# Optimization experiments

Hardware: AMD Instinct MI355X
Metric: run time of the kernel (lower is better)

## Reference

```python
import jax, jax.numpy as jnp
import numpy as np

D_MODEL = 1024
NUM_HEADS = 16
D_HEAD = D_MODEL // NUM_HEADS
EPS = 1e-06


def setup_inputs() -> dict:
    key = jax.random.key(0)
    ks = jax.random.split(key, 11)
    B, T = 16, 8192
    s = 1.0 / np.sqrt(D_MODEL)
    inp = {
        "query": jax.random.normal(ks[0], (B, 1, D_MODEL), jnp.float32),
        "key": jax.random.normal(ks[1], (B, T, D_MODEL), jnp.float32),
        "value": jax.random.normal(ks[2], (B, T, D_MODEL), jnp.float32),
        "Wq": jax.random.normal(ks[3], (D_MODEL, D_MODEL), jnp.float32) * s,
        "bq": jnp.zeros((D_MODEL,), jnp.float32),
        "Wk": jax.random.normal(ks[4], (D_MODEL, D_MODEL), jnp.float32) * s,
        "bk": jnp.zeros((D_MODEL,), jnp.float32),
        "Wv": jax.random.normal(ks[5], (D_MODEL, D_MODEL), jnp.float32) * s,
        "bv": jnp.zeros((D_MODEL,), jnp.float32),
        "Wo": jax.random.normal(ks[6], (D_MODEL, D_MODEL), jnp.float32) * s,
        "bo": jnp.zeros((D_MODEL,), jnp.float32),
    }
    return inp


def _feature_map(x):
    # ELU + 1 ensures positivity
    return jax.nn.elu(x) + 1.0


def reference(query, key, value, Wq, bq, Wk, bk, Wv, bv, Wo, bo):
    B, T, _ = key.shape
    H, dh = NUM_HEADS, D_HEAD
    # projections (torch Linear: x @ W^T + b)
    Q = (query @ Wq.T + bq).reshape(B, 1, H, dh).transpose(0, 2, 1, 3)  # [B,H,1,dh]
    K = (key @ Wk.T + bk).reshape(B, T, H, dh).transpose(0, 2, 1, 3)    # [B,H,T,dh]
    V = (value @ Wv.T + bv).reshape(B, T, H, dh).transpose(0, 2, 1, 3)  # [B,H,T,dh]
    Q = _feature_map(Q)
    K = _feature_map(K)
    # linear-attention accumulators
    KV = jnp.einsum("bhtd,bhte->bhde", K, V)        # [B,H,dh,dh]
    Z = K.sum(axis=2)                                  # [B,H,dh]
    num = jnp.einsum("bhqd,bhde->bhqe", Q, KV)       # [B,H,1,dh]
    den = jnp.einsum("bhqd,bhd->bhq", Q, Z)[..., None]  # [B,H,1,1]
    out = num / (den + EPS)
    out = out.transpose(0, 2, 1, 3).reshape(B, 1, D_MODEL)
    return out @ Wo.T + bo
```

## Files before the change

### kernel.cpp

```cpp
#include <hip/hip_runtime.h>


typedef __attribute__((ext_vector_type(8))) short  bf16x8;
typedef __attribute__((ext_vector_type(4))) short  bf16x4;
typedef __attribute__((ext_vector_type(4))) float  f32x4;

#define WS_QPHI 0u
#define WS_PRE  65536u
#define WS_S    131072u
#define WS_WKB  1179648u
#define WS_W    3276800u

__device__ __forceinline__ unsigned short f2bf(float f) {
  union { float f; unsigned u; } c; c.f = f;
  unsigned u = c.u;
  return (unsigned short)((u + 0x7fffu + ((u >> 16) & 1u)) >> 16);
}

__device__ __forceinline__ void gload_lds16(const void* g, void* l) {
  __builtin_amdgcn_global_load_lds((const __attribute__((address_space(1))) void*)g,
                                   (__attribute__((address_space(3))) void*)l, 16, 0, 0);
}

__global__ void k_convert_wk(const float* __restrict__ Wk, unsigned short* __restrict__ Wkb) {
  int i = blockIdx.x * 256 + threadIdx.x;
  f32x4 v = ((const f32x4*)Wk)[i];
  bf16x4 o;
  o[0] = (short)f2bf(v[0]); o[1] = (short)f2bf(v[1]);
  o[2] = (short)f2bf(v[2]); o[3] = (short)f2bf(v[3]);
  ((bf16x4*)Wkb)[i] = o;
}

__global__ void k_qproj(const float* __restrict__ q, const float* __restrict__ Wq,
                        const float* __restrict__ bq, float* __restrict__ Qphi) {
  int b = blockIdx.x, h = blockIdx.y, d = threadIdx.x;
  const f32x4* qr = (const f32x4*)(q + b * 1024);
  const f32x4* wr = (const f32x4*)(Wq + (size_t)(h * 64 + d) * 1024);
  float s = bq[h * 64 + d];
  for (int i = 0; i < 256; ++i) {
    f32x4 a = qr[i], ww = wr[i];
    s += a[0]*ww[0] + a[1]*ww[1] + a[2]*ww[2] + a[3]*ww[3];
  }
  s = s > 0.f ? s + 1.f : __expf(s);
  Qphi[(b * 16 + h) * 64 + d] = s;
}

__global__ __launch_bounds__(512)
void k_kproj(const float* __restrict__ key, const unsigned short* __restrict__ Wkb,
             const float* __restrict__ bk, const float* __restrict__ Qphi,
             float* __restrict__ w) {
  __shared__ unsigned short sA[2][128 * 40];
  __shared__ unsigned short sB[2][256 * 32];

  const int bid  = blockIdx.x + (blockIdx.y << 2);
  const int work = ((bid & 7) << 9) | (bid >> 3);
  const int np   = work & 3;
  const int mb   = work >> 2;
  const int b    = mb >> 6;
  const int mrow = (mb & 63) << 7;
  const int tid  = threadIdx.x;
  const int lane = tid & 63;
  const int wv   = tid >> 6;
  const int wr   = wv >> 2;
  const int wc   = wv & 3;
  const int n0   = np << 8;
  const int h    = (np << 2) | wc;
  const int l15  = lane & 15;
  const int lk   = (lane >> 4) << 3;

  const int ar = tid >> 2, aq = tid & 3;
  const float* Ab = key + ((size_t)((b << 13) + mrow + ar)) * 1024 + aq * 8;
  const int sAoff = ar * 40 + aq * 8;

  const int bsw = ((lane & 3) ^ ((lane >> 3) & 3)) << 3;
  const unsigned short* Bb = Wkb + ((size_t)(n0 + (wv << 5) + (lane >> 2))) * 1024 + bsw;

  f32x4 acc[4][4];
  #pragma unroll
  for (int i = 0; i < 4; ++i)
    #pragma unroll
    for (int j = 0; j < 4; ++j) acc[i][j] = (f32x4)0.f;

  float qreg[4];
  #pragma unroll
  for (int ni = 0; ni < 4; ++ni)
    qreg[ni] = Qphi[((b << 4) + h) * 64 + ni * 16 + l15];

  const int fsw = (l15 >> 1) & 3;

  f32x4 p0 = *(const f32x4*)(Ab);
  f32x4 p1 = *(const f32x4*)(Ab + 4);
  gload_lds16(Bb,             &sB[0][wv * 1024]);
  gload_lds16(Bb + 16 * 1024, &sB[0][wv * 1024 + 512]);
  {
    bf16x8 v;
    v[0]=(short)f2bf(p0[0]); v[1]=(short)f2bf(p0[1]); v[2]=(short)f2bf(p0[2]); v[3]=(short)f2bf(p0[3]);
    v[4]=(short)f2bf(p1[0]); v[5]=(short)f2bf(p1[1]); v[6]=(short)f2bf(p1[2]); v[7]=(short)f2bf(p1[3]);
    *(bf16x8*)&sA[0][sAoff] = v;
  }
  __syncthreads();

  for (int t = 0; t < 32; ++t) {
    const int cur = t & 1, nxt = cur ^ 1;
    f32x4 a0, a1;
    if (t < 31) {
      const float* An = Ab + (t + 1) * 32;
      a0 = *(const f32x4*)(An);
      a1 = *(const f32x4*)(An + 4);
      const unsigned short* Bn = Bb + (t + 1) * 32;
      gload_lds16(Bn,             &sB[nxt][wv * 1024]);
      gload_lds16(Bn + 16 * 1024, &sB[nxt][wv * 1024 + 512]);
    }
    bf16x8 af[4], bfr[4];
    #pragma unroll
    for (int mi = 0; mi < 4; ++mi)
      af[mi] = *(const bf16x8*)&sA[cur][((wr << 6) + mi * 16 + l15) * 40 + lk];
    #pragma unroll
    for (int ni = 0; ni < 4; ++ni)
      bfr[ni] = *(const bf16x8*)&sB[cur][((wc << 6) + ni * 16 + l15) * 32
                                         + ((((lane >> 4) ^ fsw)) << 3)];
    #pragma unroll
    for (int mi = 0; mi < 4; ++mi)
      #pragma unroll
      for (int ni = 0; ni < 4; ++ni)
        acc[mi][ni] = __builtin_amdgcn_mfma_f32_16x16x32_bf16(af[mi], bfr[ni], acc[mi][ni], 0, 0, 0);
    if (t < 31) {
      bf16x8 v;
      v[0]=(short)f2bf(a0[0]); v[1]=(short)f2bf(a0[1]); v[2]=(short)f2bf(a0[2]); v[3]=(short)f2bf(a0[3]);
      v[4]=(short)f2bf(a1[0]); v[5]=(short)f2bf(a1[1]); v[6]=(short)f2bf(a1[2]); v[7]=(short)f2bf(a1[3]);
      *(bf16x8*)&sA[nxt][sAoff] = v;
    }
    __syncthreads();
  }

  float bias[4];
  #pragma unroll
  for (int ni = 0; ni < 4; ++ni) bias[ni] = bk[n0 + (wc << 6) + ni * 16 + l15];

  #pragma unroll
  for (int mi = 0; mi < 4; ++mi) {
    float wa[4];
    #pragma unroll
    for (int r = 0; r < 4; ++r) {
      float s = 0.f;
      #pragma unroll
      for (int ni = 0; ni < 4; ++ni) {
        float x = acc[mi][ni][r] + bias[ni];
        x = x > 0.f ? x + 1.f : __expf(x);
        s += x * qreg[ni];
      }
      wa[r] = s;
    }
    #pragma unroll
    for (int m = 1; m < 16; m <<= 1)
      #pragma unroll
      for (int r = 0; r < 4; ++r) wa[r] += __shfl_xor(wa[r], m, 64);
    if (l15 == 0) {
      const int rg = lane >> 4;
      #pragma unroll
      for (int r = 0; r < 4; ++r) {
        int trow = mrow + (wr << 6) + mi * 16 + (rg << 2) + r;
        w[(((size_t)((b << 4) + h)) << 13) + trow] = wa[r];
      }
    }
  }
}

__global__ __launch_bounds__(256)
void k_sgemm(const float* __restrict__ value, const float* __restrict__ w,
             float* __restrict__ S) {
  __shared__ float wl[16 * 256];
  const int b = blockIdx.x, tc = blockIdx.y;
  const int t0 = tc << 8;
  const int tid = threadIdx.x;
  for (int i = tid; i < 16 * 256; i += 256)
    wl[i] = w[(((size_t)(b * 16 + (i >> 8))) << 13) + t0 + (i & 255)];
  __syncthreads();
  f32x4 acc[16];
  #pragma unroll
  for (int h = 0; h < 16; ++h) acc[h] = (f32x4)0.f;
  const f32x4* vb = (const f32x4*)(value + ((size_t)(b << 13) + t0) * 1024) + tid;
  #pragma unroll 4
  for (int t = 0; t < 256; ++t) {
    f32x4 x = vb[t << 8];
    #pragma unroll
    for (int h = 0; h < 16; ++h)
      acc[h] += x * wl[(h << 8) + t];
  }
  #pragma unroll
  for (int h = 0; h < 16; ++h) {
    float* sp = S + ((b << 4) + h) * 1024 + (tid << 2);
    atomicAdd(sp + 0, acc[h][0]); atomicAdd(sp + 1, acc[h][1]);
    atomicAdd(sp + 2, acc[h][2]); atomicAdd(sp + 3, acc[h][3]);
  }
}

__global__ void k_numden(const float* __restrict__ w, const float* __restrict__ S,
                         const float* __restrict__ Wv, const float* __restrict__ bv,
                         float* __restrict__ pre) {
  const int b = blockIdx.x, h = blockIdx.y, e = threadIdx.x;
  const float* wb = w + (((size_t)(b * 16 + h)) << 13);
  float dsum = 0.f;
  for (int i = 0; i < 128; ++i) dsum += wb[i * 64 + e];
  #pragma unroll
  for (int m = 1; m < 64; m <<= 1) dsum += __shfl_xor(dsum, m, 64);
  const f32x4* sr  = (const f32x4*)(S + (b * 16 + h) * 1024);
  const f32x4* wvr = (const f32x4*)(Wv + (size_t)(h * 64 + e) * 1024);
  float ns = 0.f;
  for (int i = 0; i < 256; ++i) {
    f32x4 a = sr[i], c = wvr[i];
    ns += a[0]*c[0] + a[1]*c[1] + a[2]*c[2] + a[3]*c[3];
  }
  ns += dsum * bv[h * 64 + e];
  pre[b * 1024 + h * 64 + e] = ns / (dsum + 1e-6f);
}

__global__ __launch_bounds__(256)
void k_outproj(const float* __restrict__ pre, const float* __restrict__ Wo,
               const float* __restrict__ bo, float* __restrict__ out) {
  __shared__ float pl[1024];
  const int b = blockIdx.x, ch = blockIdx.y;
  const int tid = threadIdx.x, lane = tid & 63, wv = tid >> 6;
  for (int i = tid; i < 1024; i += 256) pl[i] = pre[b * 1024 + i];
  __syncthreads();
  for (int oi = 0; oi < 64; ++oi) {
    int o = (ch << 8) + (wv << 6) + oi;
    const f32x4* wrow = (const f32x4*)(Wo + (size_t)o * 1024);
    float s = 0.f;
    #pragma unroll
    for (int j = 0; j < 4; ++j) {
      f32x4 v = wrow[lane * 4 + j];
      f32x4 p = *(const f32x4*)&pl[(lane * 4 + j) * 4];
      s += v[0]*p[0] + v[1]*p[1] + v[2]*p[2] + v[3]*p[3];
    }
    #pragma unroll
    for (int m = 1; m < 64; m <<= 1) s += __shfl_xor(s, m, 64);
    if (lane == 0) out[b * 1024 + o] = s + bo[o];
  }
}

extern "C" void kernel_launch(void* const* d_in, const int* in_sizes, int n_in,
                              void* d_out, int out_size, void* d_ws, size_t ws_size,
                              hipStream_t stream) {
  const float* query = (const float*)d_in[0];
  const float* key   = (const float*)d_in[1];
  const float* value = (const float*)d_in[2];
  const float* Wq    = (const float*)d_in[3];
  const float* bq    = (const float*)d_in[4];
  const float* Wk    = (const float*)d_in[5];
  const float* bk    = (const float*)d_in[6];
  const float* Wv    = (const float*)d_in[7];
  const float* bv    = (const float*)d_in[8];
  const float* Wo    = (const float*)d_in[9];
  const float* bo    = (const float*)d_in[10];
  float* out = (float*)d_out;
  char* ws = (char*)d_ws;
  float*          Qphi = (float*)(ws + WS_QPHI);
  float*          pre  = (float*)(ws + WS_PRE);
  float*          S    = (float*)(ws + WS_S);
  unsigned short* Wkb  = (unsigned short*)(ws + WS_WKB);
  float*          w    = (float*)(ws + WS_W);

  hipMemsetAsync(S, 0, 16 * 16 * 1024 * sizeof(float), stream);
  k_convert_wk<<<1024, 256, 0, stream>>>(Wk, Wkb);
  k_qproj<<<dim3(16, 16), 64, 0, stream>>>(query, Wq, bq, Qphi);
  k_kproj<<<dim3(4, 1024), 512, 0, stream>>>(key, Wkb, bk, Qphi, w);
  k_sgemm<<<dim3(16, 32), 256, 0, stream>>>(value, w, S);
  k_numden<<<dim3(16, 16), 64, 0, stream>>>(w, S, Wv, bv, pre);
  k_outproj<<<dim3(16, 4), 256, 0, stream>>>(pre, Wo, bo, out);
}
```

Baseline: 725.6 us.

## Stream fp32 key tiles directly to LDS with triple buffering and convert on read

The key operand is now loaded with global_load_lds straight into a triple-buffered fp32 LDS tile (XOR-swizzled), prefetched two steps ahead, instead of going through registers and being converted to bf16 before the LDS store. Conversion to bf16 now happens after the LDS read, using the packed v_cvt_pk_bf16_f32 instruction. Explicit vmcnt waits and raw barriers replace __syncthreads, and launch bounds request 4 blocks per CU. This aims to hide global-load latency and cut VGPR pressure, at the cost of doubling LDS footprint for A and doing conversion redundantly per wave.

```diff
diff --git a/kernel.cpp b/kernel.cpp
--- a/kernel.cpp
+++ b/kernel.cpp
@@ -15,6 +15,12 @@
   union { float f; unsigned u; } c; c.f = f;
   unsigned u = c.u;
   return (unsigned short)((u + 0x7fffu + ((u >> 16) & 1u)) >> 16);
+}
+
+__device__ __forceinline__ unsigned cvt_pk_bf16(float lo, float hi) {
+  unsigned r;
+  asm("v_cvt_pk_bf16_f32 %0, %1, %2" : "=v"(r) : "v"(lo), "v"(hi));
+  return r;
 }
 
 __device__ __forceinline__ void gload_lds16(const void* g, void* l) {
@@ -45,12 +51,12 @@
   Qphi[(b * 16 + h) * 64 + d] = s;
 }
 
-__global__ __launch_bounds__(512)
+__global__ __launch_bounds__(512, 4)
 void k_kproj(const float* __restrict__ key, const unsigned short* __restrict__ Wkb,
              const float* __restrict__ bk, const float* __restrict__ Qphi,
              float* __restrict__ w) {
-  __shared__ unsigned short sA[2][128 * 40];
-  __shared__ unsigned short sB[2][256 * 32];
+  __shared__ float          sAf[3][128 * 32];
+  __shared__ unsigned short sB [2][256 * 32];
 
   const int bid  = blockIdx.x + (blockIdx.y << 2);
   const int work = ((bid & 7) << 9) | (bid >> 3);
@@ -66,14 +72,19 @@
   const int n0   = np << 8;
   const int h    = (np << 2) | wc;
   const int l15  = lane & 15;
-  const int lk   = (lane >> 4) << 3;
-
-  const int ar = tid >> 2, aq = tid & 3;
-  const float* Ab = key + ((size_t)((b << 13) + mrow + ar)) * 1024 + aq * 8;
-  const int sAoff = ar * 40 + aq * 8;
+
+  const int c0    = (lane >> 4) << 1;
+  const int rx7   = l15 & 7;
+  const int cAoff = ((c0 ^ rx7) << 2);
+  const int cBoff = (((c0 + 1) ^ rx7) << 2);
+
+  const int Rr0 = (wv << 4) + (lane >> 3);
+  const int asw = ((lane & 7) ^ ((lane >> 3) & 7)) << 2;
+  const float* PA0 = key + (size_t)((b << 13) + mrow + Rr0) * 1024 + asw;
 
   const int bsw = ((lane & 3) ^ ((lane >> 3) & 3)) << 3;
   const unsigned short* Bb = Wkb + ((size_t)(n0 + (wv << 5) + (lane >> 2))) * 1024 + bsw;
+  const int fsw = (l15 >> 1) & 3;
 
   f32x4 acc[4][4];
   #pragma unroll
@@ -86,51 +97,56 @@
   for (int ni = 0; ni < 4; ++ni)
     qreg[ni] = Qphi[((b << 4) + h) * 64 + ni * 16 + l15];
 
-  const int fsw = (l15 >> 1) & 3;
-
-  f32x4 p0 = *(const f32x4*)(Ab);
-  f32x4 p1 = *(const f32x4*)(Ab + 4);
   gload_lds16(Bb,             &sB[0][wv * 1024]);
   gload_lds16(Bb + 16 * 1024, &sB[0][wv * 1024 + 512]);
-  {
-    bf16x8 v;
-    v[0]=(short)f2bf(p0[0]); v[1]=(short)f2bf(p0[1]); v[2]=(short)f2bf(p0[2]); v[3]=(short)f2bf(p0[3]);
-    v[4]=(short)f2bf(p1[0]); v[5]=(short)f2bf(p1[1]); v[6]=(short)f2bf(p1[2]); v[7]=(short)f2bf(p1[3]);
-    *(bf16x8*)&sA[0][sAoff] = v;
-  }
-  __syncthreads();
-
+  gload_lds16(PA0,            &sAf[0][(wv << 9)]);
+  gload_lds16(PA0 + 8 * 1024, &sAf[0][(wv << 9) + 256]);
+  gload_lds16(PA0 + 32,            &sAf[1][(wv << 9)]);
+  gload_lds16(PA0 + 8 * 1024 + 32, &sAf[1][(wv << 9) + 256]);
+  asm volatile("s_waitcnt vmcnt(2)" ::: "memory");
+  __builtin_amdgcn_s_barrier();
+
+  int aCur = 0;
+  #pragma unroll 1
   for (int t = 0; t < 32; ++t) {
-    const int cur = t & 1, nxt = cur ^ 1;
-    f32x4 a0, a1;
+    const int aN2 = (aCur >= 1) ? (aCur - 1) : 2;
     if (t < 31) {
-      const float* An = Ab + (t + 1) * 32;
-      a0 = *(const f32x4*)(An);
-      a1 = *(const f32x4*)(An + 4);
       const unsigned short* Bn = Bb + (t + 1) * 32;
-      gload_lds16(Bn,             &sB[nxt][wv * 1024]);
-      gload_lds16(Bn + 16 * 1024, &sB[nxt][wv * 1024 + 512]);
-    }
-    bf16x8 af[4], bfr[4];
-    #pragma unroll
-    for (int mi = 0; mi < 4; ++mi)
-      af[mi] = *(const bf16x8*)&sA[cur][((wr << 6) + mi * 16 + l15) * 40 + lk];
-    #pragma unroll
-    for (int ni = 0; ni < 4; ++ni)
-      bfr[ni] = *(const bf16x8*)&sB[cur][((wc << 6) + ni * 16 + l15) * 32
-                                         + ((((lane >> 4) ^ fsw)) << 3)];
-    #pragma unroll
-    for (int mi = 0; mi < 4; ++mi)
+      gload_lds16(Bn,             &sB[(t + 1) & 1][wv * 1024]);
+      gload_lds16(Bn + 16 * 1024, &sB[(t + 1) & 1][wv * 1024 + 512]);
+    }
+    if (t < 30) {
+      const float* An = PA0 + (t + 2) * 32;
+      gload_lds16(An,             &sAf[aN2][(wv << 9)]);
+      gload_lds16(An + 8 * 1024,  &sAf[aN2][(wv << 9) + 256]);
+    }
+    {
+      const float*          pA = &sAf[aCur][0];
+      const unsigned short* pB = &sB[t & 1][0];
+      bf16x8 bfr[4];
       #pragma unroll
       for (int ni = 0; ni < 4; ++ni)
-        acc[mi][ni] = __builtin_amdgcn_mfma_f32_16x16x32_bf16(af[mi], bfr[ni], acc[mi][ni], 0, 0, 0);
+        bfr[ni] = *(const bf16x8*)&pB[((wc << 6) + ni * 16 + l15) * 32
+                                      + (((lane >> 4) ^ fsw) << 3)];
+      #pragma unroll
+      for (int mi = 0; mi < 4; ++mi) {
+        const int rbase = ((wr << 6) + mi * 16 + l15) * 32;
+        f32x4 ca = *(const f32x4*)&pA[rbase + cAoff];
+        f32x4 cb = *(const f32x4*)&pA[rbase + cBoff];
+        union { bf16x8 v; unsigned u[4]; } af;
+        af.u[0] = cvt_pk_bf16(ca[0], ca[1]); af.u[1] = cvt_pk_bf16(ca[2], ca[3]);
+        af.u[2] = cvt_pk_bf16(cb[0], cb[1]); af.u[3] = cvt_pk_bf16(cb[2], cb[3]);
+        #pragma unroll
+        for (int ni = 0; ni < 4; ++ni)
+          acc[mi][ni] = __builtin_amdgcn_mfma_f32_16x16x32_bf16(af.v, bfr[ni], acc[mi][ni], 0, 0, 0);
+      }
+    }
     if (t < 31) {
-      bf16x8 v;
-      v[0]=(short)f2bf(a0[0]); v[1]=(short)f2bf(a0[1]); v[2]=(short)f2bf(a0[2]); v[3]=(short)f2bf(a0[3]);
-      v[4]=(short)f2bf(a1[0]); v[5]=(short)f2bf(a1[1]); v[6]=(short)f2bf(a1[2]); v[7]=(short)f2bf(a1[3]);
-      *(bf16x8*)&sA[nxt][sAoff] = v;
-    }
-    __syncthreads();
+      if (t < 30) asm volatile("s_waitcnt vmcnt(2) lgkmcnt(0)" ::: "memory");
+      else        asm volatile("s_waitcnt vmcnt(0) lgkmcnt(0)" ::: "memory");
+      __builtin_amdgcn_s_barrier();
+    }
+    aCur = (aCur == 2) ? 0 : aCur + 1;
   }
 
   float bias[4];
```

New measurement: 699.4 us. -3.6%, faster.

## Triple-buffer K-projection B tiles, use packed bf16 convert, widen small tail kernels

Applied to the files above, without the earlier changes.

The K-projection GEMM now triple-buffers the weight tiles in LDS and issues global-to-LDS loads two iterations ahead. It replaces __syncthreads with explicit waitcnt plus s_barrier under sched_barrier fences, and converts fp32 to bf16 with the hardware v_cvt_pk_bf16_f32 instruction instead of manual rounding. The numden kernel splits its reductions across four waves with an LDS combine, and outproj launches twice as many blocks with half the rows each. The aim is to hide load latency in the dominant GEMM and add parallelism to the tail kernels, at the cost of extra LDS, fragile manual wait counts, and a launch bound that may limit registers.

```diff
diff --git a/kernel.cpp b/kernel.cpp
--- a/kernel.cpp
+++ b/kernel.cpp
@@ -15,6 +15,19 @@
   union { float f; unsigned u; } c; c.f = f;
   unsigned u = c.u;
   return (unsigned short)((u + 0x7fffu + ((u >> 16) & 1u)) >> 16);
+}
+
+__device__ __forceinline__ unsigned cvt_pk_bf16(float lo, float hi) {
+  unsigned r;
+  asm("v_cvt_pk_bf16_f32 %0, %1, %2" : "=v"(r) : "v"(lo), "v"(hi));
+  return r;
+}
+
+__device__ __forceinline__ uint4 pack_bf16x8(f32x4 x, f32x4 y) {
+  uint4 r;
+  r.x = cvt_pk_bf16(x[0], x[1]); r.y = cvt_pk_bf16(x[2], x[3]);
+  r.z = cvt_pk_bf16(y[0], y[1]); r.w = cvt_pk_bf16(y[2], y[3]);
+  return r;
 }
 
 __device__ __forceinline__ void gload_lds16(const void* g, void* l) {
@@ -45,12 +58,12 @@
   Qphi[(b * 16 + h) * 64 + d] = s;
 }
 
-__global__ __launch_bounds__(512)
+__global__ __launch_bounds__(512, 4)
 void k_kproj(const float* __restrict__ key, const unsigned short* __restrict__ Wkb,
              const float* __restrict__ bk, const float* __restrict__ Qphi,
              float* __restrict__ w) {
-  __shared__ unsigned short sA[2][128 * 40];
-  __shared__ unsigned short sB[2][256 * 32];
+  __shared__ __align__(16) unsigned short sA[2][128 * 40];
+  __shared__ __align__(16) unsigned short sB[3][256 * 32];
 
   const int bid  = blockIdx.x + (blockIdx.y << 2);
   const int work = ((bid & 7) << 9) | (bid >> 3);
@@ -74,6 +87,7 @@
 
   const int bsw = ((lane & 3) ^ ((lane >> 3) & 3)) << 3;
   const unsigned short* Bb = Wkb + ((size_t)(n0 + (wv << 5) + (lane >> 2))) * 1024 + bsw;
+  const int fsw = (l15 >> 1) & 3;
 
   f32x4 acc[4][4];
   #pragma unroll
@@ -86,51 +100,59 @@
   for (int ni = 0; ni < 4; ++ni)
     qreg[ni] = Qphi[((b << 4) + h) * 64 + ni * 16 + l15];
 
-  const int fsw = (l15 >> 1) & 3;
-
-  f32x4 p0 = *(const f32x4*)(Ab);
-  f32x4 p1 = *(const f32x4*)(Ab + 4);
-  gload_lds16(Bb,             &sB[0][wv * 1024]);
-  gload_lds16(Bb + 16 * 1024, &sB[0][wv * 1024 + 512]);
-  {
-    bf16x8 v;
-    v[0]=(short)f2bf(p0[0]); v[1]=(short)f2bf(p0[1]); v[2]=(short)f2bf(p0[2]); v[3]=(short)f2bf(p0[3]);
-    v[4]=(short)f2bf(p1[0]); v[5]=(short)f2bf(p1[1]); v[6]=(short)f2bf(p1[2]); v[7]=(short)f2bf(p1[3]);
-    *(bf16x8*)&sA[0][sAoff] = v;
-  }
-  __syncthreads();
-
+  f32x4 a0 = *(const f32x4*)(Ab);
+  f32x4 a1 = *(const f32x4*)(Ab + 4);
+  __builtin_amdgcn_sched_barrier(0);
+  gload_lds16(Bb,                  &sB[0][wv * 1024]);
+  gload_lds16(Bb + 16 * 1024,      &sB[0][wv * 1024 + 512]);
+  gload_lds16(Bb + 32,             &sB[1][wv * 1024]);
+  gload_lds16(Bb + 16 * 1024 + 32, &sB[1][wv * 1024 + 512]);
+  __builtin_amdgcn_sched_barrier(0);
+  *(uint4*)&sA[0][sAoff] = pack_bf16x8(a0, a1);
+  asm volatile("s_waitcnt vmcnt(2) lgkmcnt(0)" ::: "memory");
+  __builtin_amdgcn_s_barrier();
+  __builtin_amdgcn_sched_barrier(0);
+
+  #pragma unroll 1
   for (int t = 0; t < 32; ++t) {
-    const int cur = t & 1, nxt = cur ^ 1;
-    f32x4 a0, a1;
     if (t < 31) {
       const float* An = Ab + (t + 1) * 32;
       a0 = *(const f32x4*)(An);
       a1 = *(const f32x4*)(An + 4);
-      const unsigned short* Bn = Bb + (t + 1) * 32;
-      gload_lds16(Bn,             &sB[nxt][wv * 1024]);
-      gload_lds16(Bn + 16 * 1024, &sB[nxt][wv * 1024 + 512]);
-    }
-    bf16x8 af[4], bfr[4];
-    #pragma unroll
-    for (int mi = 0; mi < 4; ++mi)
-      af[mi] = *(const bf16x8*)&sA[cur][((wr << 6) + mi * 16 + l15) * 40 + lk];
-    #pragma unroll
-    for (int ni = 0; ni < 4; ++ni)
-      bfr[ni] = *(const bf16x8*)&sB[cur][((wc << 6) + ni * 16 + l15) * 32
-                                         + ((((lane >> 4) ^ fsw)) << 3)];
-    #pragma unroll
-    for (int mi = 0; mi < 4; ++mi)
+    }
+    __builtin_amdgcn_sched_barrier(0);
+    if (t < 30) {
+      const unsigned short* Bn = Bb + (t + 2) * 32;
+      const int bn = (t + 2) % 3;
+      gload_lds16(Bn,             &sB[bn][wv * 1024]);
+      gload_lds16(Bn + 16 * 1024, &sB[bn][wv * 1024 + 512]);
+    }
+    __builtin_amdgcn_sched_barrier(0);
+    {
+      const unsigned short* pA = &sA[t & 1][0];
+      const unsigned short* pB = &sB[t % 3][0];
+      bf16x8 af[4], bfr[4];
+      #pragma unroll
+      for (int mi = 0; mi < 4; ++mi)
+        af[mi] = *(const bf16x8*)&pA[((wr << 6) + mi * 16 + l15) * 40 + lk];
       #pragma unroll
       for (int ni = 0; ni < 4; ++ni)
-        acc[mi][ni] = __builtin_amdgcn_mfma_f32_16x16x32_bf16(af[mi], bfr[ni], acc[mi][ni], 0, 0, 0);
+        bfr[ni] = *(const bf16x8*)&pB[((wc << 6) + ni * 16 + l15) * 32
+                                      + (((lane >> 4) ^ fsw) << 3)];
+      #pragma unroll
+      for (int mi = 0; mi < 4; ++mi)
+        #pragma unroll
+        for (int ni = 0; ni < 4; ++ni)
+          acc[mi][ni] = __builtin_amdgcn_mfma_f32_16x16x32_bf16(af[mi], bfr[ni], acc[mi][ni], 0, 0, 0);
+    }
+    if (t < 31)
+      *(uint4*)&sA[(t + 1) & 1][sAoff] = pack_bf16x8(a0, a1);
+    if (t < 30)      asm volatile("s_waitcnt vmcnt(2) lgkmcnt(0)" ::: "memory");
+    else if (t < 31) asm volatile("s_waitcnt vmcnt(0) lgkmcnt(0)" ::: "memory");
     if (t < 31) {
-      bf16x8 v;
-      v[0]=(short)f2bf(a0[0]); v[1]=(short)f2bf(a0[1]); v[2]=(short)f2bf(a0[2]); v[3]=(short)f2bf(a0[3]);
-      v[4]=(short)f2bf(a1[0]); v[5]=(short)f2bf(a1[1]); v[6]=(short)f2bf(a1[2]); v[7]=(short)f2bf(a1[3]);
-      *(bf16x8*)&sA[nxt][sAoff] = v;
-    }
-    __syncthreads();
+      __builtin_amdgcn_s_barrier();
+      __builtin_amdgcn_sched_barrier(0);
+    }
   }
 
   float bias[4];
@@ -195,24 +217,33 @@
   }
 }
 
-__global__ void k_numden(const float* __restrict__ w, const float* __restrict__ S,
-                         const float* __restrict__ Wv, const float* __restrict__ bv,
-                         float* __restrict__ pre) {
-  const int b = blockIdx.x, h = blockIdx.y, e = threadIdx.x;
+__global__ __launch_bounds__(256)
+void k_numden(const float* __restrict__ w, const float* __restrict__ S,
+              const float* __restrict__ Wv, const float* __restrict__ bv,
+              float* __restrict__ pre) {
+  __shared__ float red[2][4][64];
+  const int b = blockIdx.x, h = blockIdx.y;
+  const int tid = threadIdx.x, e = tid & 63, part = tid >> 6;
   const float* wb = w + (((size_t)(b * 16 + h)) << 13);
   float dsum = 0.f;
-  for (int i = 0; i < 128; ++i) dsum += wb[i * 64 + e];
-  #pragma unroll
-  for (int m = 1; m < 64; m <<= 1) dsum += __shfl_xor(dsum, m, 64);
+  for (int i = part * 32; i < part * 32 + 32; ++i) dsum += wb[i * 64 + e];
   const f32x4* sr  = (const f32x4*)(S + (b * 16 + h) * 1024);
   const f32x4* wvr = (const f32x4*)(Wv + (size_t)(h * 64 + e) * 1024);
   float ns = 0.f;
-  for (int i = 0; i < 256; ++i) {
+  for (int i = part * 64; i < part * 64 + 64; ++i) {
     f32x4 a = sr[i], c = wvr[i];
     ns += a[0]*c[0] + a[1]*c[1] + a[2]*c[2] + a[3]*c[3];
   }
-  ns += dsum * bv[h * 64 + e];
-  pre[b * 1024 + h * 64 + e] = ns / (dsum + 1e-6f);
+  red[0][part][e] = dsum; red[1][part][e] = ns;
+  __syncthreads();
+  if (part == 0) {
+    float d = red[0][0][e] + red[0][1][e] + red[0][2][e] + red[0][3][e];
+    float n = red[1][0][e] + red[1][1][e] + red[1][2][e] + red[1][3][e];
+    #pragma unroll
+    for (int m = 1; m < 64; m <<= 1) d += __shfl_xor(d, m, 64);
+    n += d * bv[h * 64 + e];
+    pre[b * 1024 + h * 64 + e] = n / (d + 1e-6f);
+  }
 }
 
 __global__ __launch_bounds__(256)
@@ -223,8 +254,8 @@
   const int tid = threadIdx.x, lane = tid & 63, wv = tid >> 6;
   for (int i = tid; i < 1024; i += 256) pl[i] = pre[b * 1024 + i];
   __syncthreads();
-  for (int oi = 0; oi < 64; ++oi) {
-    int o = (ch << 8) + (wv << 6) + oi;
+  for (int oi = 0; oi < 32; ++oi) {
+    int o = (ch << 7) + (wv << 5) + oi;
     const f32x4* wrow = (const f32x4*)(Wo + (size_t)o * 1024);
     float s = 0.f;
     #pragma unroll
@@ -266,6 +297,6 @@
   k_qproj<<<dim3(16, 16), 64, 0, stream>>>(query, Wq, bq, Qphi);
   k_kproj<<<dim3(4, 1024), 512, 0, stream>>>(key, Wkb, bk, Qphi, w);
   k_sgemm<<<dim3(16, 32), 256, 0, stream>>>(value, w, S);
-  k_numden<<<dim3(16, 16), 64, 0, stream>>>(w, S, Wv, bv, pre);
-  k_outproj<<<dim3(16, 4), 256, 0, stream>>>(pre, Wo, bo, out);
-}
+  k_numden<<<dim3(16, 16), 256, 0, stream>>>(w, S, Wv, bv, pre);
+  k_outproj<<<dim3(16, 8), 256, 0, stream>>>(pre, Wo, bo, out);
+}
```

Measured after the change: 653.1 us. 10.0% less time.
